# Kernel optimization log

Measured on AMD Instinct MI355X. Metric: run time of the kernel, lower is better.

The kernel has to match this reference:

```python
import jax, jax.numpy as jnp
import numpy as np

BLOCK_SIZE = 64          # elements per quantization block
SCALER_BLOCK_SIZE = 256  # scalers per double-quantization block
OUT, IN = 11008, 4096
N_BLOCKS = OUT * IN // BLOCK_SIZE          # 704512
N_SCALER_BLOCKS = N_BLOCKS // SCALER_BLOCK_SIZE  # 2752

# QLoRA NF4 (4-bit NormalFloat) codebook
NF4_TABLE = np.array([
    -1.0, -0.6961928009986877, -0.5250730514526367, -0.39491748809814453,
    -0.28444138169288635, -0.18477343022823334, -0.10644006729125977,
    -0.029167551919817924, 0.0, 0.07958029955625534, 0.16093020141124725,
    0.24611230194568634, 0.33791524171829224, 0.44070982933044434,
    0.5626170039176941, 0.7229568362236023], dtype=np.float32)


def setup_inputs() -> dict:
    key = jax.random.key(0)
    k1, k2, k3, k4, k5 = jax.random.split(key, 5)
    x = jax.random.normal(k1, (4, 2048, IN), dtype=jnp.float32)
    # 4-bit codebook indices for each weight element
    qweight = jax.random.randint(k2, (OUT, IN), 0, 16, dtype=jnp.int32)
    # int8-style quantized per-block scalers (positive magnitudes)
    quantized_scalers = jax.random.randint(k3, (N_BLOCKS,), 1, 127, dtype=jnp.int32)
    # per scaler-block quantization factor (strictly positive, away from zero)
    quantization_factor = jax.random.uniform(k4, (N_SCALER_BLOCKS,), dtype=jnp.float32,
                                             minval=0.5, maxval=1.5) * 127.0
    scaler_mean = jax.random.uniform(k5, (1,), dtype=jnp.float32) * 0.01
    return {"x": x, "qweight": qweight, "quantized_scalers": quantized_scalers,
            "quantization_factor": quantization_factor, "scaler_mean": scaler_mean}


def dequantize_nf4(qweight, quantized_scalers, quantization_factor, scaler_mean, dtype):
    table = jnp.asarray(NF4_TABLE, dtype=dtype)
    # double-dequantize the per-block scalers
    scalers = (quantized_scalers.astype(dtype)
               / jnp.repeat(quantization_factor.astype(dtype), SCALER_BLOCK_SIZE)
               + scaler_mean.astype(dtype)[0])                      # [N_BLOCKS]
    # codebook lookup, then per-block scale
    w = table[qweight].reshape(N_BLOCKS, BLOCK_SIZE) * scalers[:, None]
    return w.reshape(OUT, IN)


def reference(x, qweight, quantized_scalers, quantization_factor, scaler_mean):
    # Faithful to LinearNF4.forward: F.linear(x, weight.to(x.dtype))
    w = dequantize_nf4(qweight, quantized_scalers, quantization_factor,
                       scaler_mean, x.dtype)                        # [OUT, IN]
    return jnp.einsum('bsi,oi->bso', x, w)
```

## Files before the change

### kernel.cpp

```cpp
#include <hip/hip_runtime.h>
#include <stdint.h>

#define M_ROWS 8192
#define K_DIM  4096
#define N_DIM  11008
#define KSTEPS (K_DIM / 64)

#define BM 256
#define BN 256
#define MBLKS (M_ROWS / BM)
#define NBLKS (N_DIM / BN)
#define NWG   (MBLKS * NBLKS)

typedef __attribute__((ext_vector_type(4))) float          f32x4;
typedef __attribute__((ext_vector_type(8))) __bf16         bf16x8;
typedef __attribute__((ext_vector_type(4))) int            i32x4;
typedef __attribute__((ext_vector_type(8))) unsigned short u16x8;

__constant__ float NF4_TBL[16] = {
    -1.0f, -0.6961928009986877f, -0.5250730514526367f, -0.39491748809814453f,
    -0.28444138169288635f, -0.18477343022823334f, -0.10644006729125977f,
    -0.029167551919817924f, 0.0f, 0.07958029955625534f, 0.16093020141124725f,
    0.24611230194568634f, 0.33791524171829224f, 0.44070982933044434f,
    0.5626170039176941f, 0.7229568362236023f};

__device__ __forceinline__ unsigned short f2bf(float f) {
  uint32_t u = __float_as_uint(f);
  u += 0x7fffu + ((u >> 16) & 1u);
  return (unsigned short)(u >> 16);
}

__device__ __forceinline__ void gload_lds16(const void* g, const void* l) {
  __builtin_amdgcn_global_load_lds(
      (const __attribute__((address_space(1))) void*)(uintptr_t)g,
      (__attribute__((address_space(3))) void*)(uint32_t)(uintptr_t)l,
      16, 0, 0);
}

__global__ void convert_x_kernel(const float* __restrict__ x,
                                 unsigned short* __restrict__ xb) {
  const long n8 = (long)M_ROWS * K_DIM / 8;
  for (long t = (long)blockIdx.x * blockDim.x + threadIdx.x; t < n8;
       t += (long)gridDim.x * blockDim.x) {
    const float* p = x + t * 8;
    f32x4 v0 = *(const f32x4*)p;
    f32x4 v1 = *(const f32x4*)(p + 4);
    u16x8 o;
    o[0] = f2bf(v0[0]); o[1] = f2bf(v0[1]); o[2] = f2bf(v0[2]); o[3] = f2bf(v0[3]);
    o[4] = f2bf(v1[0]); o[5] = f2bf(v1[1]); o[6] = f2bf(v1[2]); o[7] = f2bf(v1[3]);
    *(u16x8*)(xb + t * 8) = o;
  }
}

__global__ void dequant_w_kernel(const int* __restrict__ qw,
                                 const int* __restrict__ qs,
                                 const float* __restrict__ qf,
                                 const float* __restrict__ mean,
                                 unsigned short* __restrict__ wb) {
  __shared__ float tbl[16];
  if (threadIdx.x < 16) tbl[threadIdx.x] = NF4_TBL[threadIdx.x];
  __syncthreads();
  const float mu = mean[0];
  const long n8 = (long)N_DIM * K_DIM / 8;
  for (long t = (long)blockIdx.x * blockDim.x + threadIdx.x; t < n8;
       t += (long)gridDim.x * blockDim.x) {
    long f = t * 8;
    int  g = (int)(f >> 6);
    float s = (float)qs[g] / qf[g >> 8] + mu;
    i32x4 q0 = *(const i32x4*)(qw + f);
    i32x4 q1 = *(const i32x4*)(qw + f + 4);
    u16x8 o;
    o[0] = f2bf(tbl[q0[0]] * s); o[1] = f2bf(tbl[q0[1]] * s);
    o[2] = f2bf(tbl[q0[2]] * s); o[3] = f2bf(tbl[q0[3]] * s);
    o[4] = f2bf(tbl[q1[0]] * s); o[5] = f2bf(tbl[q1[1]] * s);
    o[6] = f2bf(tbl[q1[2]] * s); o[7] = f2bf(tbl[q1[3]] * s);
    *(u16x8*)(wb + f) = o;
  }
}

#define STG(GP, LB)                                                              \
  gload_lds16((GP) + (long)srow * K_DIM + scol, &LDSbuf[(LB) + wid * 1024]);     \
  gload_lds16((GP) + (long)(64 + srow) * K_DIM + scol,                           \
              &LDSbuf[(LB) + 8192 + wid * 1024]);

#define SB __builtin_amdgcn_sched_barrier(0)

#define RD_A2(DST, MB, SA)                                                        \
  DST[0][0] = *(const bf16x8*)&LDSbuf[(SA) + aoff + (MB) * 2048 + kswz0];         \
  DST[0][1] = *(const bf16x8*)&LDSbuf[(SA) + aoff + (MB) * 2048 + kswz1];         \
  DST[1][0] = *(const bf16x8*)&LDSbuf[(SA) + aoff + ((MB) + 1) * 2048 + kswz0];   \
  DST[1][1] = *(const bf16x8*)&LDSbuf[(SA) + aoff + ((MB) + 1) * 2048 + kswz1];

#define RD_B2(NB, CB)                                                             \
  bq[NB][0]     = *(const bf16x8*)&LDSbuf[(CB) + boff + (NB) * 2048 + kswz0];     \
  bq[NB][1]     = *(const bf16x8*)&LDSbuf[(CB) + boff + (NB) * 2048 + kswz1];     \
  bq[NB + 1][0] = *(const bf16x8*)&LDSbuf[(CB) + boff + ((NB) + 1) * 2048 + kswz0];\
  bq[NB + 1][1] = *(const bf16x8*)&LDSbuf[(CB) + boff + ((NB) + 1) * 2048 + kswz1];

#define MFP(MI, AF, AI, NI)                                                       \
  acc[MI][NI] = __builtin_amdgcn_mfma_f32_16x16x32_bf16(AF[AI][0], bq[NI][0], acc[MI][NI], 0, 0, 0); \
  acc[MI][NI] = __builtin_amdgcn_mfma_f32_16x16x32_bf16(AF[AI][1], bq[NI][1], acc[MI][NI], 0, 0, 0);

__global__ __launch_bounds__(512, 2) void gemm_pipe(
    const unsigned short* __restrict__ xb, const unsigned short* __restrict__ wb,
    float* __restrict__ C) {
  __align__(16) __shared__ unsigned char LDSbuf[163840];

  const int tid = threadIdx.x;
  const int wid = tid >> 6, lane = tid & 63;
  const int wr = wid >> 2, wc = wid & 3;
  const int r16 = lane & 15, hi = lane >> 4;

  const int p = ((int)blockIdx.x & 7) * (NWG / 8) + ((int)blockIdx.x >> 3);
  int mb, nb;
  if (p < 1280) {
    const int nbg = p >> 7;
    const int rem = p & 127;
    const int mbg = rem >> 5;
    const int s   = rem & 31;
    mb = mbg * 8 + (s & 7);
    nb = nbg * 4 + (s >> 3);
  } else {
    const int q   = p - 1280;
    const int mbg = q / 24;
    const int s   = q % 24;
    mb = mbg * 8 + (s & 7);
    nb = 40 + (s >> 3);
  }
  const long m0g = (long)mb * BM, n0g = (long)nb * BN;

  const int srow = wid * 8 + (lane >> 3);
  const int scol = ((lane & 7) ^ (lane >> 3)) * 8;

  const int aoff = (wr * 128 + r16) * 128;
  const int boff = (wc * 64 + r16) * 128;
  const int kswz0 = ((hi ^ (r16 & 7)) << 4);
  const int kswz1 = kswz0 ^ 64;

  STG(xb + m0g * K_DIM,              0);
  STG(xb + (m0g + 128) * K_DIM,      16384);
  STG(wb + n0g * K_DIM,              98304);
  STG(wb + (n0g + 128) * K_DIM,      98304 + 16384);
  STG(xb + m0g * K_DIM + 64,         32768);
  STG(xb + (m0g + 128) * K_DIM + 64, 32768 + 16384);
  asm volatile("s_waitcnt vmcnt(4)");
  __builtin_amdgcn_sched_barrier(0);
  __builtin_amdgcn_s_barrier();

  bf16x8 af_a[2][2], af_b[2][2], bq[4][2];
  f32x4 acc[8][4] = {};

  int sAr = 0, sAn = 32768, sAs = 65536;

  for (int t = 0; t < KSTEPS; ++t) {
    const int cur = t & 1;
    const int cB = 98304 + cur * 32768;
    const int nB = 98304 + (cur ^ 1) * 32768;
    const long kB = (long)((t + 1 < KSTEPS ? t + 1 : KSTEPS - 1) * 64);
    const long kA = (long)((t + 2 < KSTEPS ? t + 2 : KSTEPS - 1) * 64);

    RD_A2(af_a, 0, sAr);
    RD_B2(0, cB);
    SB;
    RD_B2(2, cB);
    STG(wb + n0g * K_DIM + kB, nB);
    __builtin_amdgcn_s_setprio(1);
    MFP(0, af_a, 0, 0) MFP(1, af_a, 1, 0) MFP(0, af_a, 0, 1) MFP(1, af_a, 1, 1)
    __builtin_amdgcn_s_setprio(0);
    SB;
    RD_A2(af_b, 2, sAr);
    STG(wb + (n0g + 128) * K_DIM + kB, nB + 16384);
    __builtin_amdgcn_s_setprio(1);
    MFP(0, af_a, 0, 2) MFP(1, af_a, 1, 2) MFP(0, af_a, 0, 3) MFP(1, af_a, 1, 3)
    __builtin_amdgcn_s_setprio(0);
    SB;
    STG(xb + m0g * K_DIM + kA, sAs);
    __builtin_amdgcn_s_setprio(1);
    MFP(2, af_b, 0, 2) MFP(3, af_b, 1, 2) MFP(2, af_b, 0, 3) MFP(3, af_b, 1, 3)
    __builtin_amdgcn_s_setprio(0);
    SB;
    RD_A2(af_a, 4, sAr);
    STG(xb + (m0g + 128) * K_DIM + kA, sAs + 16384);
    __builtin_amdgcn_s_setprio(1);
    MFP(2, af_b, 0, 0) MFP(3, af_b, 1, 0) MFP(2, af_b, 0, 1) MFP(3, af_b, 1, 1)
    __builtin_amdgcn_s_setprio(0);
    SB;
    __builtin_amdgcn_s_setprio(1);
    MFP(4, af_a, 0, 0) MFP(5, af_a, 1, 0) MFP(4, af_a, 0, 1) MFP(5, af_a, 1, 1)
    __builtin_amdgcn_s_setprio(0);
    SB;
    RD_A2(af_b, 6, sAr);
    __builtin_amdgcn_s_setprio(1);
    MFP(4, af_a, 0, 2) MFP(5, af_a, 1, 2) MFP(4, af_a, 0, 3) MFP(5, af_a, 1, 3)
    __builtin_amdgcn_s_setprio(0);
    SB;
    __builtin_amdgcn_s_setprio(1);
    MFP(6, af_b, 0, 2) MFP(7, af_b, 1, 2) MFP(6, af_b, 0, 3) MFP(7, af_b, 1, 3)
    __builtin_amdgcn_s_setprio(0);
    SB;
    __builtin_amdgcn_s_setprio(1);
    MFP(6, af_b, 0, 0) MFP(7, af_b, 1, 0) MFP(6, af_b, 0, 1) MFP(7, af_b, 1, 1)
    __builtin_amdgcn_s_setprio(0);
    asm volatile("s_waitcnt vmcnt(4)");
    __builtin_amdgcn_sched_barrier(0);
    __builtin_amdgcn_s_barrier();
    __builtin_amdgcn_sched_barrier(0);

    int tmp = sAr; sAr = sAn; sAn = sAs; sAs = tmp;
  }

  const long crow = m0g + wr * 128 + hi * 4;
  const long ccol = n0g + wc * 64 + r16;
#pragma unroll
  for (int m = 0; m < 8; ++m)
#pragma unroll
    for (int n = 0; n < 4; ++n)
#pragma unroll
      for (int r = 0; r < 4; ++r)
        __builtin_nontemporal_store(
            acc[m][n][r], &C[(crow + m * 16 + r) * N_DIM + ccol + n * 16]);
}

__global__ __launch_bounds__(256) void gemm_fallback(
    const float* __restrict__ Xf, const int* __restrict__ qw,
    const int* __restrict__ qs, const float* __restrict__ qf,
    const float* __restrict__ meanp, float* __restrict__ C) {
  __shared__ unsigned short As[128 * 64];
  __shared__ unsigned short Bs[128 * 64];
  __shared__ float tbl[16];
  const int tid = threadIdx.x;
  if (tid < 16) tbl[tid] = NF4_TBL[tid];
  const float mu = meanp[0];
  const int nwg = (M_ROWS / 128) * (N_DIM / 128);
  const int wg = ((int)blockIdx.x & 7) * (nwg / 8) + ((int)blockIdx.x >> 3);
  const int mbf = wg % (M_ROWS / 128), nbf = wg / (M_ROWS / 128);
  const int m0 = mbf * 128, n0 = nbf * 128;
  const int wid = tid >> 6, lane = tid & 63;
  const int wrf = wid >> 1, wcc = wid & 1;
  const int r16 = lane & 15, hi = lane >> 4;
  f32x4 acc[4][4] = {};
  for (int t = 0; t < KSTEPS; ++t) {
    const int k0 = t * 64;
    __syncthreads();
#pragma unroll
    for (int i = 0; i < 4; ++i) {
      int gi = i * 256 + tid;
      int row = gi >> 3, kq = (gi & 7) * 8;
      const float* px = Xf + (long)(m0 + row) * K_DIM + k0 + kq;
      f32x4 v0 = *(const f32x4*)px;
      f32x4 v1 = *(const f32x4*)(px + 4);
      u16x8 o;
      o[0] = f2bf(v0[0]); o[1] = f2bf(v0[1]); o[2] = f2bf(v0[2]); o[3] = f2bf(v0[3]);
      o[4] = f2bf(v1[0]); o[5] = f2bf(v1[1]); o[6] = f2bf(v1[2]); o[7] = f2bf(v1[3]);
      *(u16x8*)&As[row * 64 + kq] = o;
    }
#pragma unroll
    for (int i = 0; i < 4; ++i) {
      int gi = i * 256 + tid;
      int row = gi >> 3, kq = (gi & 7) * 8;
      const int* pq = qw + (long)(n0 + row) * K_DIM + k0 + kq;
      i32x4 q0 = *(const i32x4*)pq;
      i32x4 q1 = *(const i32x4*)(pq + 4);
      int g = (n0 + row) * (K_DIM / 64) + t;
      float s = (float)qs[g] / qf[g >> 8] + mu;
      u16x8 o;
      o[0] = f2bf(tbl[q0[0]] * s); o[1] = f2bf(tbl[q0[1]] * s);
      o[2] = f2bf(tbl[q0[2]] * s); o[3] = f2bf(tbl[q0[3]] * s);
      o[4] = f2bf(tbl[q1[0]] * s); o[5] = f2bf(tbl[q1[1]] * s);
      o[6] = f2bf(tbl[q1[2]] * s); o[7] = f2bf(tbl[q1[3]] * s);
      *(u16x8*)&Bs[row * 64 + kq] = o;
    }
    __syncthreads();
    bf16x8 afr[4][2], bfr[4][2];
#pragma unroll
    for (int i = 0; i < 4; ++i)
#pragma unroll
      for (int h = 0; h < 2; ++h) {
        afr[i][h] = *(const bf16x8*)&As[(wrf * 64 + i * 16 + r16) * 64 + h * 32 + hi * 8];
        bfr[i][h] = *(const bf16x8*)&Bs[(wcc * 64 + i * 16 + r16) * 64 + h * 32 + hi * 8];
      }
#pragma unroll
    for (int i = 0; i < 4; ++i)
#pragma unroll
      for (int j = 0; j < 4; ++j) {
        acc[i][j] = __builtin_amdgcn_mfma_f32_16x16x32_bf16(afr[i][0], bfr[j][0], acc[i][j], 0, 0, 0);
        acc[i][j] = __builtin_amdgcn_mfma_f32_16x16x32_bf16(afr[i][1], bfr[j][1], acc[i][j], 0, 0, 0);
      }
  }
  const int crow = m0 + wrf * 64 + hi * 4;
  const int ccol = n0 + wcc * 64 + r16;
#pragma unroll
  for (int i = 0; i < 4; ++i)
#pragma unroll
    for (int j = 0; j < 4; ++j)
#pragma unroll
      for (int r = 0; r < 4; ++r)
        C[(long)(crow + i * 16 + r) * N_DIM + (ccol + j * 16)] = acc[i][j][r];
}

extern "C" void kernel_launch(void* const* d_in, const int* in_sizes, int n_in,
                              void* d_out, int out_size, void* d_ws, size_t ws_size,
                              hipStream_t stream) {
  const float* x    = (const float*)d_in[0];
  const int*   qw   = (const int*)d_in[1];
  const int*   qs   = (const int*)d_in[2];
  const float* qf   = (const float*)d_in[3];
  const float* mean = (const float*)d_in[4];
  float* out = (float*)d_out;

  const size_t xb_bytes = (size_t)M_ROWS * K_DIM * 2;
  const size_t wb_bytes = (size_t)N_DIM * K_DIM * 2;

  if (ws_size >= xb_bytes + wb_bytes) {
    unsigned short* xb = (unsigned short*)d_ws;
    unsigned short* wb = (unsigned short*)((char*)d_ws + xb_bytes);
    convert_x_kernel<<<4096, 256, 0, stream>>>(x, xb);
    dequant_w_kernel<<<4096, 256, 0, stream>>>(qw, qs, qf, mean, wb);
    gemm_pipe<<<NWG, 512, 0, stream>>>(xb, wb, out);
  } else {
    gemm_fallback<<<(M_ROWS / 128) * (N_DIM / 128), 256, 0, stream>>>(
        x, qw, qs, qf, mean, out);
  }
}
```

Measured before the change: 693.4 us.

## Use 4 waves per workgroup with 128x128 per-wave output tiles

Shrinks the GEMM workgroup from 8 waves to 4. Each wave now computes a 128x128 output tile (8x8 MFMA accumulators) instead of 128x64, and the cooperative global-to-LDS staging issues four loads per wave instead of two. The aim is more MFMA work per LDS fragment read and fewer waves contending at barriers. In exchange, accumulator register use doubles (256 VGPRs of accumulators), which risks spills and leaves fewer waves to hide memory latency.

```diff
diff --git a/kernel.cpp b/kernel.cpp
--- a/kernel.cpp
+++ b/kernel.cpp
@@ -79,9 +79,14 @@
 }
 
 #define STG(GP, LB)                                                              \
-  gload_lds16((GP) + (long)srow * K_DIM + scol, &LDSbuf[(LB) + wid * 1024]);     \
-  gload_lds16((GP) + (long)(64 + srow) * K_DIM + scol,                           \
-              &LDSbuf[(LB) + 8192 + wid * 1024]);
+  gload_lds16((GP) + (long)srow * K_DIM + scol,                                  \
+              &LDSbuf[(LB) + wid * 1024]);                                       \
+  gload_lds16((GP) + (long)(srow + 32) * K_DIM + scol,                           \
+              &LDSbuf[(LB) + wid * 1024 + 4096]);                                \
+  gload_lds16((GP) + (long)(srow + 64) * K_DIM + scol,                           \
+              &LDSbuf[(LB) + wid * 1024 + 8192]);                                \
+  gload_lds16((GP) + (long)(srow + 96) * K_DIM + scol,                           \
+              &LDSbuf[(LB) + wid * 1024 + 12288]);
 
 #define SB __builtin_amdgcn_sched_barrier(0)
 
@@ -91,24 +96,36 @@
   DST[1][0] = *(const bf16x8*)&LDSbuf[(SA) + aoff + ((MB) + 1) * 2048 + kswz0];   \
   DST[1][1] = *(const bf16x8*)&LDSbuf[(SA) + aoff + ((MB) + 1) * 2048 + kswz1];
 
-#define RD_B2(NB, CB)                                                             \
-  bq[NB][0]     = *(const bf16x8*)&LDSbuf[(CB) + boff + (NB) * 2048 + kswz0];     \
-  bq[NB][1]     = *(const bf16x8*)&LDSbuf[(CB) + boff + (NB) * 2048 + kswz1];     \
-  bq[NB + 1][0] = *(const bf16x8*)&LDSbuf[(CB) + boff + ((NB) + 1) * 2048 + kswz0];\
-  bq[NB + 1][1] = *(const bf16x8*)&LDSbuf[(CB) + boff + ((NB) + 1) * 2048 + kswz1];
+#define RD_B4(N0, CB)                                                             \
+  bq[(N0) + 0][0] = *(const bf16x8*)&LDSbuf[(CB) + boff + ((N0) + 0) * 2048 + kswz0]; \
+  bq[(N0) + 0][1] = *(const bf16x8*)&LDSbuf[(CB) + boff + ((N0) + 0) * 2048 + kswz1]; \
+  bq[(N0) + 1][0] = *(const bf16x8*)&LDSbuf[(CB) + boff + ((N0) + 1) * 2048 + kswz0]; \
+  bq[(N0) + 1][1] = *(const bf16x8*)&LDSbuf[(CB) + boff + ((N0) + 1) * 2048 + kswz1]; \
+  bq[(N0) + 2][0] = *(const bf16x8*)&LDSbuf[(CB) + boff + ((N0) + 2) * 2048 + kswz0]; \
+  bq[(N0) + 2][1] = *(const bf16x8*)&LDSbuf[(CB) + boff + ((N0) + 2) * 2048 + kswz1]; \
+  bq[(N0) + 3][0] = *(const bf16x8*)&LDSbuf[(CB) + boff + ((N0) + 3) * 2048 + kswz0]; \
+  bq[(N0) + 3][1] = *(const bf16x8*)&LDSbuf[(CB) + boff + ((N0) + 3) * 2048 + kswz1];
 
 #define MFP(MI, AF, AI, NI)                                                       \
   acc[MI][NI] = __builtin_amdgcn_mfma_f32_16x16x32_bf16(AF[AI][0], bq[NI][0], acc[MI][NI], 0, 0, 0); \
   acc[MI][NI] = __builtin_amdgcn_mfma_f32_16x16x32_bf16(AF[AI][1], bq[NI][1], acc[MI][NI], 0, 0, 0);
 
-__global__ __launch_bounds__(512, 2) void gemm_pipe(
+#define CL(MB, AF, N0)                                                            \
+  __builtin_amdgcn_s_setprio(1);                                                  \
+  MFP((MB) + 0, AF, 0, (N0) + 0) MFP((MB) + 1, AF, 1, (N0) + 0)                   \
+  MFP((MB) + 0, AF, 0, (N0) + 1) MFP((MB) + 1, AF, 1, (N0) + 1)                   \
+  MFP((MB) + 0, AF, 0, (N0) + 2) MFP((MB) + 1, AF, 1, (N0) + 2)                   \
+  MFP((MB) + 0, AF, 0, (N0) + 3) MFP((MB) + 1, AF, 1, (N0) + 3)                   \
+  __builtin_amdgcn_s_setprio(0);
+
+__global__ __launch_bounds__(256, 1) void gemm_pipe(
     const unsigned short* __restrict__ xb, const unsigned short* __restrict__ wb,
     float* __restrict__ C) {
   __align__(16) __shared__ unsigned char LDSbuf[163840];
 
   const int tid = threadIdx.x;
   const int wid = tid >> 6, lane = tid & 63;
-  const int wr = wid >> 2, wc = wid & 3;
+  const int wr = wid >> 1, wc = wid & 1;
   const int r16 = lane & 15, hi = lane >> 4;
 
   const int p = ((int)blockIdx.x & 7) * (NWG / 8) + ((int)blockIdx.x >> 3);
@@ -133,7 +150,7 @@
   const int scol = ((lane & 7) ^ (lane >> 3)) * 8;
 
   const int aoff = (wr * 128 + r16) * 128;
-  const int boff = (wc * 64 + r16) * 128;
+  const int boff = (wc * 128 + r16) * 128;
   const int kswz0 = ((hi ^ (r16 & 7)) << 4);
   const int kswz1 = kswz0 ^ 64;
 
@@ -143,12 +160,12 @@
   STG(wb + (n0g + 128) * K_DIM,      98304 + 16384);
   STG(xb + m0g * K_DIM + 64,         32768);
   STG(xb + (m0g + 128) * K_DIM + 64, 32768 + 16384);
-  asm volatile("s_waitcnt vmcnt(4)");
+  asm volatile("s_waitcnt vmcnt(8)");
   __builtin_amdgcn_sched_barrier(0);
   __builtin_amdgcn_s_barrier();
 
-  bf16x8 af_a[2][2], af_b[2][2], bq[4][2];
-  f32x4 acc[8][4] = {};
+  bf16x8 af_a[2][2], af_b[2][2], bq[8][2];
+  f32x4 acc[8][8] = {};
 
   int sAr = 0, sAn = 32768, sAs = 65536;
 
@@ -160,48 +177,32 @@
     const long kA = (long)((t + 2 < KSTEPS ? t + 2 : KSTEPS - 1) * 64);
 
     RD_A2(af_a, 0, sAr);
-    RD_B2(0, cB);
-    SB;
-    RD_B2(2, cB);
+    RD_B4(0, cB);
+    SB;
+    RD_B4(4, cB);
     STG(wb + n0g * K_DIM + kB, nB);
-    __builtin_amdgcn_s_setprio(1);
-    MFP(0, af_a, 0, 0) MFP(1, af_a, 1, 0) MFP(0, af_a, 0, 1) MFP(1, af_a, 1, 1)
-    __builtin_amdgcn_s_setprio(0);
+    CL(0, af_a, 0)
     SB;
     RD_A2(af_b, 2, sAr);
     STG(wb + (n0g + 128) * K_DIM + kB, nB + 16384);
-    __builtin_amdgcn_s_setprio(1);
-    MFP(0, af_a, 0, 2) MFP(1, af_a, 1, 2) MFP(0, af_a, 0, 3) MFP(1, af_a, 1, 3)
-    __builtin_amdgcn_s_setprio(0);
-    SB;
+    CL(0, af_a, 4)
+    SB;
+    RD_A2(af_a, 4, sAr);
     STG(xb + m0g * K_DIM + kA, sAs);
-    __builtin_amdgcn_s_setprio(1);
-    MFP(2, af_b, 0, 2) MFP(3, af_b, 1, 2) MFP(2, af_b, 0, 3) MFP(3, af_b, 1, 3)
-    __builtin_amdgcn_s_setprio(0);
-    SB;
-    RD_A2(af_a, 4, sAr);
+    CL(2, af_b, 0)
+    SB;
     STG(xb + (m0g + 128) * K_DIM + kA, sAs + 16384);
-    __builtin_amdgcn_s_setprio(1);
-    MFP(2, af_b, 0, 0) MFP(3, af_b, 1, 0) MFP(2, af_b, 0, 1) MFP(3, af_b, 1, 1)
-    __builtin_amdgcn_s_setprio(0);
-    SB;
-    __builtin_amdgcn_s_setprio(1);
-    MFP(4, af_a, 0, 0) MFP(5, af_a, 1, 0) MFP(4, af_a, 0, 1) MFP(5, af_a, 1, 1)
-    __builtin_amdgcn_s_setprio(0);
+    CL(2, af_b, 4)
     SB;
     RD_A2(af_b, 6, sAr);
-    __builtin_amdgcn_s_setprio(1);
-    MFP(4, af_a, 0, 2) MFP(5, af_a, 1, 2) MFP(4, af_a, 0, 3) MFP(5, af_a, 1, 3)
-    __builtin_amdgcn_s_setprio(0);
-    SB;
-    __builtin_amdgcn_s_setprio(1);
-    MFP(6, af_b, 0, 2) MFP(7, af_b, 1, 2) MFP(6, af_b, 0, 3) MFP(7, af_b, 1, 3)
-    __builtin_amdgcn_s_setprio(0);
-    SB;
-    __builtin_amdgcn_s_setprio(1);
-    MFP(6, af_b, 0, 0) MFP(7, af_b, 1, 0) MFP(6, af_b, 0, 1) MFP(7, af_b, 1, 1)
-    __builtin_amdgcn_s_setprio(0);
-    asm volatile("s_waitcnt vmcnt(4)");
+    CL(4, af_a, 0)
+    SB;
+    CL(4, af_a, 4)
+    SB;
+    CL(6, af_b, 0)
+    SB;
+    CL(6, af_b, 4)
+    asm volatile("s_waitcnt vmcnt(8)");
     __builtin_amdgcn_sched_barrier(0);
     __builtin_amdgcn_s_barrier();
     __builtin_amdgcn_sched_barrier(0);
@@ -210,11 +211,11 @@
   }
 
   const long crow = m0g + wr * 128 + hi * 4;
-  const long ccol = n0g + wc * 64 + r16;
+  const long ccol = n0g + wc * 128 + r16;
 #pragma unroll
   for (int m = 0; m < 8; ++m)
 #pragma unroll
-    for (int n = 0; n < 4; ++n)
+    for (int n = 0; n < 8; ++n)
 #pragma unroll
       for (int r = 0; r < 4; ++r)
         __builtin_nontemporal_store(
@@ -316,7 +317,7 @@
     unsigned short* wb = (unsigned short*)((char*)d_ws + xb_bytes);
     convert_x_kernel<<<4096, 256, 0, stream>>>(x, xb);
     dequant_w_kernel<<<4096, 256, 0, stream>>>(qw, qs, qf, mean, wb);
-    gemm_pipe<<<NWG, 512, 0, stream>>>(xb, wb, out);
+    gemm_pipe<<<NWG, 256, 0, stream>>>(xb, wb, out);
   } else {
     gemm_fallback<<<(M_ROWS / 128) * (N_DIM / 128), 256, 0, stream>>>(
         x, qw, qs, qf, mean, out);
```

Measured after the change: 737.6 us. 1.06x slower.
